# Kernel tuning notes

Measured on AMD Instinct MI355X. Metric: run time of the kernel, lower is better.

## Reference

```python
import jax, jax.numpy as jnp
import numpy as np

EMBED_DIM = 1024
NUM_HEADS = 16
HEAD_DIM = EMBED_DIM // NUM_HEADS
BATCH = 4
SEQ = 2048


def setup_inputs() -> dict:
    key = jax.random.key(0)
    ks = jax.random.split(key, 9)
    s = 1.0 / np.sqrt(EMBED_DIM)
    return {
        "query": jax.random.normal(ks[0], (BATCH, SEQ, EMBED_DIM), jnp.float32),
        "Wq": jax.random.normal(ks[1], (EMBED_DIM, EMBED_DIM), jnp.float32) * s,
        "bq": jnp.zeros((EMBED_DIM,), jnp.float32),
        "Wk": jax.random.normal(ks[2], (EMBED_DIM, EMBED_DIM), jnp.float32) * s,
        "bk": jnp.zeros((EMBED_DIM,), jnp.float32),
        "Wv": jax.random.normal(ks[3], (EMBED_DIM, EMBED_DIM), jnp.float32) * s,
        "bv": jnp.zeros((EMBED_DIM,), jnp.float32),
        "Wo": jax.random.normal(ks[4], (EMBED_DIM, EMBED_DIM), jnp.float32) * s,
        "bo": jnp.zeros((EMBED_DIM,), jnp.float32),
    }


def reference(query, Wq, bq, Wk, bk, Wv, bv, Wo, bo):
    bsz, seq, embed_dim = query.shape
    scaling = HEAD_DIM ** (-0.5)
    # projections (torch Linear: x @ W.T + b)
    q = (query @ Wq.T + bq) * scaling
    k = query @ Wk.T + bk
    v = query @ Wv.T + bv
    # [b, h, s, d]
    q = q.reshape(bsz, seq, NUM_HEADS, HEAD_DIM).transpose(0, 2, 1, 3)
    k = k.reshape(bsz, seq, NUM_HEADS, HEAD_DIM).transpose(0, 2, 1, 3)
    v = v.reshape(bsz, seq, NUM_HEADS, HEAD_DIM).transpose(0, 2, 1, 3)
    # full [b, h, s, s] scores (faithful to the naive original)
    scores = jnp.einsum("bhqd,bhkd->bhqk", q, k)
    causal = jnp.tril(jnp.ones((seq, seq), bool))  # [s, s]
    scores = jnp.where(causal[None, None], scores, -jnp.inf)
    probs = jax.nn.softmax(scores, axis=-1)
    attn = jnp.einsum("bhqk,bhkd->bhqd", probs, v)
    attn = attn.transpose(0, 2, 1, 3).reshape(bsz, seq, embed_dim)
    return attn @ Wo.T + bo
```

## Files before the change

kernel.cpp:

```cpp
#include <hip/hip_runtime.h>
#include <stdint.h>

typedef unsigned short u16;
typedef __attribute__((ext_vector_type(8))) __bf16 bf16x8;
typedef __attribute__((ext_vector_type(4))) float f32x4;

#define SEQL 2048
#define NHEADS 16
#define HDIM 64
#define BSZ 4
#define EMB 1024
#define MROWS (BSZ * SEQL)
#define LOG2E 1.44269504088896f

__device__ __forceinline__ u16 f2bf(float f) {
  union { float f; uint32_t u; } v; v.f = f;
  return (u16)((v.u + 0x7fffu + ((v.u >> 16) & 1u)) >> 16);
}

__device__ __forceinline__ void gload_lds16(const u16* g, u16* l) {
  __builtin_amdgcn_global_load_lds(
      (__attribute__((address_space(1))) void*)(g),
      (__attribute__((address_space(3))) void*)(l), 16, 0, 0);
}

__device__ __forceinline__ void cvt8(const float* __restrict__ in, u16* __restrict__ out, int i) {
  float4 a = *(const float4*)(in + i);
  float4 b = *(const float4*)(in + i + 4);
  uint4 o;
  o.x = f2bf(a.x) | ((uint32_t)f2bf(a.y) << 16);
  o.y = f2bf(a.z) | ((uint32_t)f2bf(a.w) << 16);
  o.z = f2bf(b.x) | ((uint32_t)f2bf(b.y) << 16);
  o.w = f2bf(b.z) | ((uint32_t)f2bf(b.w) << 16);
  *(uint4*)(out + i) = o;
}

__global__ void cvt_kernel(const float* __restrict__ in, u16* __restrict__ out, int n) {
  int i = (blockIdx.x * blockDim.x + threadIdx.x) * 8;
  if (i + 8 <= n) cvt8(in, out, i);
}

__global__ void cvt_w4(const float* __restrict__ w0, const float* __restrict__ w1,
                       const float* __restrict__ w2, const float* __restrict__ w3,
                       u16* __restrict__ o0, u16* __restrict__ o1,
                       u16* __restrict__ o2, u16* __restrict__ o3) {
  const float* in = blockIdx.y == 0 ? w0 : blockIdx.y == 1 ? w1 : blockIdx.y == 2 ? w2 : w3;
  u16* out = blockIdx.y == 0 ? o0 : blockIdx.y == 1 ? o1 : blockIdx.y == 2 ? o2 : o3;
  int i = (blockIdx.x * blockDim.x + threadIdx.x) * 8;
  cvt8(in, out, i);
}

__device__ __forceinline__ void gemm_core(const u16* __restrict__ A, const u16* __restrict__ B,
                                          int m0, int n0, u16* As, u16* Bs, f32x4 acc[4][4]) {
  const int tid = threadIdx.x;
  const int lane = tid & 63;
  const int wid = tid >> 6;
  const int wm = wid >> 1, wn = wid & 1;
  const int srow = lane >> 2;
  const int scol = (lane & 3) * 8;
  const int lrow = lane & 15;
  const int kg = (lane >> 4) * 8;

  const u16* Ag0 = A + (size_t)(m0 + wid * 32 + srow) * EMB + scol;
  const u16* Bg0 = B + (size_t)(n0 + wid * 32 + srow) * EMB + scol;
  u16* Al0 = As + (wid * 32 + srow) * 32 + scol;
  u16* Bl0 = Bs + (wid * 32 + srow) * 32 + scol;

  for (int k0 = 0; k0 < EMB; k0 += 32) {
    gload_lds16(Ag0 + k0, Al0);
    gload_lds16(Ag0 + k0 + 16 * EMB, Al0 + 16 * 32);
    gload_lds16(Bg0 + k0, Bl0);
    gload_lds16(Bg0 + k0 + 16 * EMB, Bl0 + 16 * 32);
    __syncthreads();
    bf16x8 af[4], bfr[4];
#pragma unroll
    for (int f = 0; f < 4; ++f) {
      af[f]  = *(const bf16x8*)(As + (wm * 64 + f * 16 + lrow) * 32 + kg);
      bfr[f] = *(const bf16x8*)(Bs + (wn * 64 + f * 16 + lrow) * 32 + kg);
    }
#pragma unroll
    for (int fm = 0; fm < 4; ++fm)
#pragma unroll
      for (int fn = 0; fn < 4; ++fn)
        acc[fm][fn] = __builtin_amdgcn_mfma_f32_16x16x32_bf16(af[fm], bfr[fn], acc[fm][fn], 0, 0, 0);
    __syncthreads();
  }
}

__global__ __launch_bounds__(256, 2) void gemm_qkv(
    const u16* __restrict__ X,
    const u16* __restrict__ Wq, const u16* __restrict__ Wk, const u16* __restrict__ Wv,
    const float* __restrict__ bq, const float* __restrict__ bk, const float* __restrict__ bv,
    u16* __restrict__ Qb, u16* __restrict__ Kb, u16* __restrict__ Vt) {
  __shared__ u16 As[128 * 32];
  __shared__ u16 Bs[128 * 32];
  const int which = blockIdx.y;
  const u16* W = which == 0 ? Wq : which == 1 ? Wk : Wv;
  const float* bias = which == 0 ? bq : which == 1 ? bk : bv;

  const int mt = blockIdx.x >> 3, nt = blockIdx.x & 7;
  const f32x4 fzero = {0.f, 0.f, 0.f, 0.f};
  f32x4 acc[4][4];
#pragma unroll
  for (int i = 0; i < 4; ++i)
#pragma unroll
    for (int j = 0; j < 4; ++j) acc[i][j] = fzero;

  gemm_core(X, W, mt * 128, nt * 128, As, Bs, acc);

  const int lane = threadIdx.x & 63;
  const int wid = threadIdx.x >> 6;
  const int wm = wid >> 1, wn = wid & 1;
  const int lrow = lane & 15, g = lane >> 4;

  if (which == 2) {
#pragma unroll
    for (int fm = 0; fm < 4; ++fm)
#pragma unroll
      for (int fn = 0; fn < 4; ++fn) {
        int n = nt * 128 + wn * 64 + fn * 16 + lrow;
        float bs = bias[n];
        int h = n >> 6, d = n & 63;
        int m0 = mt * 128 + wm * 64 + fm * 16 + g * 4;
        int b = m0 >> 11, s = m0 & 2047;
        union { u16 s4[4]; uint2 u; } o;
#pragma unroll
        for (int r = 0; r < 4; ++r) o.s4[r] = f2bf(acc[fm][fn][r] + bs);
        *(uint2*)(Vt + ((size_t)(b * NHEADS + h) * HDIM + d) * SEQL + s) = o.u;
      }
  } else {
    u16* Ob = which == 0 ? Qb : Kb;
    const float scale = which == 0 ? 0.125f * LOG2E : 1.0f;
#pragma unroll
    for (int fm = 0; fm < 4; ++fm)
#pragma unroll
      for (int fn = 0; fn < 4; ++fn) {
        int n = nt * 128 + wn * 64 + fn * 16 + lrow;
        float bs = bias[n];
        int h = n >> 6, d = n & 63;
#pragma unroll
        for (int r = 0; r < 4; ++r) {
          int m = mt * 128 + wm * 64 + fm * 16 + g * 4 + r;
          int b = m >> 11, s = m & 2047;
          float v = (acc[fm][fn][r] + bs) * scale;
          Ob[(size_t)((b * NHEADS + h) * SEQL + s) * HDIM + d] = f2bf(v);
        }
      }
  }
}

__global__ __launch_bounds__(256, 2) void gemm_out(
    const u16* __restrict__ Ain, const u16* __restrict__ Wo,
    const float* __restrict__ bo, float* __restrict__ out) {
  __shared__ u16 As[128 * 32];
  __shared__ u16 Bs[128 * 32];
  const int mt = blockIdx.x >> 3, nt = blockIdx.x & 7;
  const f32x4 fzero = {0.f, 0.f, 0.f, 0.f};
  f32x4 acc[4][4];
#pragma unroll
  for (int i = 0; i < 4; ++i)
#pragma unroll
    for (int j = 0; j < 4; ++j) acc[i][j] = fzero;

  gemm_core(Ain, Wo, mt * 128, nt * 128, As, Bs, acc);

  const int lane = threadIdx.x & 63;
  const int wid = threadIdx.x >> 6;
  const int wm = wid >> 1, wn = wid & 1;
  const int lrow = lane & 15, g = lane >> 4;
#pragma unroll
  for (int fm = 0; fm < 4; ++fm)
#pragma unroll
    for (int fn = 0; fn < 4; ++fn) {
      int n = nt * 128 + wn * 64 + fn * 16 + lrow;
      float bs = bo[n];
#pragma unroll
      for (int r = 0; r < 4; ++r) {
        int m = mt * 128 + wm * 64 + fm * 16 + g * 4 + r;
        out[(size_t)m * EMB + n] = acc[fm][fn][r] + bs;
      }
    }
}

__device__ __forceinline__ int swz(int row, int colE) {
  return row * 64 + (colE ^ ((row & 7) << 3));
}

__global__ __launch_bounds__(256, 4) void attn2_kernel(
    const u16* __restrict__ Qb, const u16* __restrict__ Kb, const u16* __restrict__ Vt,
    u16* __restrict__ Ab) {
  __shared__ u16 Ks[2][64 * 64];
  __shared__ u16 Vs[2][64 * 64];

  const int bid = blockIdx.x;
  const int grp = bid >> 6;
  const int bh  = bid & 63;
  const int qt  = (grp & 1) ? (grp >> 1) : (31 - (grp >> 1));
  const int q0  = qt * 64;
  const int NT  = qt + 1;

  const int tid = threadIdx.x, lane = tid & 63, wid = tid >> 6;
  const int lrow = lane & 15, g = lane >> 4, kg = g * 8;

  const u16* Qbh = Qb + (size_t)bh * SEQL * HDIM;
  const u16* Kbh = Kb + (size_t)bh * SEQL * HDIM;
  const u16* Vbh = Vt + (size_t)bh * HDIM * SEQL;

  const int qrow = q0 + wid * 16 + lrow;
  const bf16x8 qf0 = *(const bf16x8*)(Qbh + (size_t)qrow * HDIM + kg);
  const bf16x8 qf1 = *(const bf16x8*)(Qbh + (size_t)qrow * HDIM + 32 + kg);

  const int srow = tid >> 3;
  const int sce  = (tid & 7) * 8;

  float m_run = -1e30f, l_run = 0.f;
  const f32x4 fzero = {0.f, 0.f, 0.f, 0.f};
  f32x4 accO[4];
#pragma unroll
  for (int d = 0; d < 4; ++d) accO[d] = fzero;

  {
    uint4 k0 = *(const uint4*)(Kbh + (size_t)srow * HDIM + sce);
    uint4 k1 = *(const uint4*)(Kbh + (size_t)(srow + 32) * HDIM + sce);
    uint4 v0 = *(const uint4*)(Vbh + (size_t)srow * SEQL + sce);
    uint4 v1 = *(const uint4*)(Vbh + (size_t)(srow + 32) * SEQL + sce);
    *(uint4*)(&Ks[0][swz(srow, sce)]) = k0;
    *(uint4*)(&Ks[0][swz(srow + 32, sce)]) = k1;
    *(uint4*)(&Vs[0][swz(srow, sce)]) = v0;
    *(uint4*)(&Vs[0][swz(srow + 32, sce)]) = v1;
  }
  __syncthreads();

  for (int t = 0; t < NT; ++t) {
    const int cur = t & 1;
    const int kv0 = t * 64;
    const bool pf = (t + 1 < NT);
    uint4 k0, k1, v0, v1;
    if (pf) {
      const int kvn = kv0 + 64;
      k0 = *(const uint4*)(Kbh + (size_t)(kvn + srow) * HDIM + sce);
      k1 = *(const uint4*)(Kbh + (size_t)(kvn + srow + 32) * HDIM + sce);
      v0 = *(const uint4*)(Vbh + (size_t)srow * SEQL + kvn + sce);
      v1 = *(const uint4*)(Vbh + (size_t)(srow + 32) * SEQL + kvn + sce);
    }

    f32x4 sacc[4];
    __builtin_amdgcn_s_setprio(1);
#pragma unroll
    for (int kb = 0; kb < 4; ++kb) {
      bf16x8 kfa = *(const bf16x8*)(&Ks[cur][swz(kb * 16 + lrow, kg)]);
      bf16x8 kfb = *(const bf16x8*)(&Ks[cur][swz(kb * 16 + lrow, 32 + kg)]);
      f32x4 z = fzero;
      z = __builtin_amdgcn_mfma_f32_16x16x32_bf16(kfa, qf0, z, 0, 0, 0);
      z = __builtin_amdgcn_mfma_f32_16x16x32_bf16(kfb, qf1, z, 0, 0, 0);
      sacc[kb] = z;
    }
    __builtin_amdgcn_s_setprio(0);

    if (kv0 + 63 > q0 + wid * 16) {
#pragma unroll
      for (int kb = 0; kb < 4; ++kb)
#pragma unroll
        for (int r = 0; r < 4; ++r)
          if (kv0 + kb * 16 + g * 4 + r > qrow) sacc[kb][r] = -1e30f;
    }

    float mx = sacc[0][0];
#pragma unroll
    for (int kb = 0; kb < 4; ++kb)
#pragma unroll
      for (int r = 0; r < 4; ++r) mx = fmaxf(mx, sacc[kb][r]);
    mx = fmaxf(mx, __shfl_xor(mx, 16));
    mx = fmaxf(mx, __shfl_xor(mx, 32));

    if (!__all(mx <= m_run + 8.f)) {
      const float mnew = fmaxf(m_run, mx);
      const float sc = __builtin_amdgcn_exp2f(m_run - mnew);
      m_run = mnew;
      l_run *= sc;
#pragma unroll
      for (int d = 0; d < 4; ++d) accO[d] *= sc;
    }

    bf16x8 pa[2];
    float ls = 0.f;
#pragma unroll
    for (int kb = 0; kb < 4; ++kb)
#pragma unroll
      for (int r = 0; r < 4; ++r) {
        float p = __builtin_amdgcn_exp2f(sacc[kb][r] - m_run);
        ls += p;
        pa[kb >> 1][(kb & 1) * 4 + r] = (__bf16)p;
      }
    l_run += ls;

    __builtin_amdgcn_s_setprio(1);
#pragma unroll
    for (int ks = 0; ks < 2; ++ks)
#pragma unroll
      for (int d = 0; d < 4; ++d) {
        union { ushort4 h[2]; bf16x8 v; } vf;
        vf.h[0] = *(const ushort4*)(&Vs[cur][swz(d * 16 + lrow, ks * 32 + g * 4)]);
        vf.h[1] = *(const ushort4*)(&Vs[cur][swz(d * 16 + lrow, ks * 32 + 16 + g * 4)]);
        accO[d] = __builtin_amdgcn_mfma_f32_16x16x32_bf16(vf.v, pa[ks], accO[d], 0, 0, 0);
      }
    __builtin_amdgcn_s_setprio(0);

    if (pf) {
      const int nb = cur ^ 1;
      *(uint4*)(&Ks[nb][swz(srow, sce)]) = k0;
      *(uint4*)(&Ks[nb][swz(srow + 32, sce)]) = k1;
      *(uint4*)(&Vs[nb][swz(srow, sce)]) = v0;
      *(uint4*)(&Vs[nb][swz(srow + 32, sce)]) = v1;
    }
    __syncthreads();
  }

  float l = l_run;
  l += __shfl_xor(l, 16);
  l += __shfl_xor(l, 32);
  const float inv = 1.f / l;
  const int b = bh >> 4, h = bh & 15;
#pragma unroll
  for (int d = 0; d < 4; ++d) {
    union { u16 s4[4]; uint2 u; } o;
#pragma unroll
    for (int r = 0; r < 4; ++r) o.s4[r] = f2bf(accO[d][r] * inv);
    *(uint2*)(Ab + (size_t)(b * SEQL + qrow) * EMB + h * HDIM + d * 16 + g * 4) = o.u;
  }
}

extern "C" void kernel_launch(void* const* d_in, const int* in_sizes, int n_in,
                              void* d_out, int out_size, void* d_ws, size_t ws_size,
                              hipStream_t stream) {
  (void)in_sizes; (void)n_in; (void)out_size; (void)ws_size;
  const float* query = (const float*)d_in[0];
  const float* Wq = (const float*)d_in[1];
  const float* bq = (const float*)d_in[2];
  const float* Wk = (const float*)d_in[3];
  const float* bk = (const float*)d_in[4];
  const float* Wv = (const float*)d_in[5];
  const float* bv = (const float*)d_in[6];
  const float* Wo = (const float*)d_in[7];
  const float* bo = (const float*)d_in[8];
  float* out = (float*)d_out;

  const size_t MB = 1u << 20;
  char* ws = (char*)d_ws;
  u16* Xb  = (u16*)(ws);
  u16* Wqb = (u16*)(ws + 16 * MB);
  u16* Wkb = (u16*)(ws + 18 * MB);
  u16* Wvb = (u16*)(ws + 20 * MB);
  u16* Wob = (u16*)(ws + 22 * MB);
  u16* Qbf = (u16*)(ws + 24 * MB);
  u16* Kbf = (u16*)(ws + 40 * MB);
  u16* Vtg = (u16*)(ws + 56 * MB);
  u16* Ab  = Xb;

  cvt_kernel<<<4096, 256, 0, stream>>>(query, Xb, MROWS * EMB);
  cvt_w4<<<dim3(512, 4), 256, 0, stream>>>(Wq, Wk, Wv, Wo, Wqb, Wkb, Wvb, Wob);
  gemm_qkv<<<dim3(512, 3), 256, 0, stream>>>(Xb, Wqb, Wkb, Wvb, bq, bk, bv, Qbf, Kbf, Vtg);
  attn2_kernel<<<2048, 256, 0, stream>>>(Qbf, Kbf, Vtg, Ab);
  gemm_out<<<512, 256, 0, stream>>>(Ab, Wob, bo, out);
}
```

Before: 191.7 us.

## Use 128-wide KV tiles in attention and merge conversion kernels into one launch

The attention kernel now processes 128 keys per iteration with a single LDS buffer instead of double-buffered 64-key tiles. This halves the loop iterations and barriers per pass and widens each softmax step, at the cost of more registers, an extra barrier around the LDS refill, and wasted masked work on the diagonal tile for odd query tiles. The two bf16 conversion kernels for activations and weights are also fused into one launch, which relies on the four weight buffers being contiguous in the workspace.

```diff
diff --git a/kernel.cpp b/kernel.cpp
--- a/kernel.cpp
+++ b/kernel.cpp
@@ -35,19 +35,21 @@
   *(uint4*)(out + i) = o;
 }
 
-__global__ void cvt_kernel(const float* __restrict__ in, u16* __restrict__ out, int n) {
+#define XN (MROWS * EMB)
+__global__ void cvt_all(const float* __restrict__ query,
+                        const float* __restrict__ w0, const float* __restrict__ w1,
+                        const float* __restrict__ w2, const float* __restrict__ w3,
+                        u16* __restrict__ Xb, u16* __restrict__ Wqb) {
   int i = (blockIdx.x * blockDim.x + threadIdx.x) * 8;
-  if (i + 8 <= n) cvt8(in, out, i);
-}
-
-__global__ void cvt_w4(const float* __restrict__ w0, const float* __restrict__ w1,
-                       const float* __restrict__ w2, const float* __restrict__ w3,
-                       u16* __restrict__ o0, u16* __restrict__ o1,
-                       u16* __restrict__ o2, u16* __restrict__ o3) {
-  const float* in = blockIdx.y == 0 ? w0 : blockIdx.y == 1 ? w1 : blockIdx.y == 2 ? w2 : w3;
-  u16* out = blockIdx.y == 0 ? o0 : blockIdx.y == 1 ? o1 : blockIdx.y == 2 ? o2 : o3;
-  int i = (blockIdx.x * blockDim.x + threadIdx.x) * 8;
-  cvt8(in, out, i);
+  if (i < XN) {
+    cvt8(query, Xb, i);
+  } else {
+    int j = i - XN;
+    int w = j >> 20;
+    int jj = j & 1048575;
+    const float* src = w == 0 ? w0 : w == 1 ? w1 : w == 2 ? w2 : w3;
+    cvt8(src, Wqb + ((size_t)w << 20), jj);
+  }
 }
 
 __device__ __forceinline__ void gemm_core(const u16* __restrict__ A, const u16* __restrict__ B,
@@ -182,22 +184,25 @@
     }
 }
 
-__device__ __forceinline__ int swz(int row, int colE) {
+__device__ __forceinline__ int swzK(int row, int colE) {
   return row * 64 + (colE ^ ((row & 7) << 3));
 }
-
-__global__ __launch_bounds__(256, 4) void attn2_kernel(
+__device__ __forceinline__ int swzV(int row, int colE) {
+  return row * 128 + (colE ^ ((row & 7) << 3));
+}
+
+__global__ __launch_bounds__(256, 4) void attn3_kernel(
     const u16* __restrict__ Qb, const u16* __restrict__ Kb, const u16* __restrict__ Vt,
     u16* __restrict__ Ab) {
-  __shared__ u16 Ks[2][64 * 64];
-  __shared__ u16 Vs[2][64 * 64];
+  __shared__ u16 Ks[128 * 64];
+  __shared__ u16 Vs[64 * 128];
 
   const int bid = blockIdx.x;
   const int grp = bid >> 6;
   const int bh  = bid & 63;
   const int qt  = (grp & 1) ? (grp >> 1) : (31 - (grp >> 1));
   const int q0  = qt * 64;
-  const int NT  = qt + 1;
+  const int NT  = (qt + 2) >> 1;
 
   const int tid = threadIdx.x, lane = tid & 63, wid = tid >> 6;
   const int lrow = lane & 15, g = lane >> 4, kg = g * 8;
@@ -210,8 +215,8 @@
   const bf16x8 qf0 = *(const bf16x8*)(Qbh + (size_t)qrow * HDIM + kg);
   const bf16x8 qf1 = *(const bf16x8*)(Qbh + (size_t)qrow * HDIM + 32 + kg);
 
-  const int srow = tid >> 3;
-  const int sce  = (tid & 7) * 8;
+  const int kr = tid >> 3, kc = (tid & 7) * 8;
+  const int vr = tid >> 4, vc = (tid & 15) * 8;
 
   float m_run = -1e30f, l_run = 0.f;
   const f32x4 fzero = {0.f, 0.f, 0.f, 0.f};
@@ -219,37 +224,34 @@
 #pragma unroll
   for (int d = 0; d < 4; ++d) accO[d] = fzero;
 
-  {
-    uint4 k0 = *(const uint4*)(Kbh + (size_t)srow * HDIM + sce);
-    uint4 k1 = *(const uint4*)(Kbh + (size_t)(srow + 32) * HDIM + sce);
-    uint4 v0 = *(const uint4*)(Vbh + (size_t)srow * SEQL + sce);
-    uint4 v1 = *(const uint4*)(Vbh + (size_t)(srow + 32) * SEQL + sce);
-    *(uint4*)(&Ks[0][swz(srow, sce)]) = k0;
-    *(uint4*)(&Ks[0][swz(srow + 32, sce)]) = k1;
-    *(uint4*)(&Vs[0][swz(srow, sce)]) = v0;
-    *(uint4*)(&Vs[0][swz(srow + 32, sce)]) = v1;
+#pragma unroll
+  for (int i = 0; i < 4; ++i) {
+    uint4 kk = *(const uint4*)(Kbh + (size_t)(kr + i * 32) * HDIM + kc);
+    *(uint4*)(&Ks[swzK(kr + i * 32, kc)]) = kk;
+    uint4 vv = *(const uint4*)(Vbh + (size_t)(vr + i * 16) * SEQL + vc);
+    *(uint4*)(&Vs[swzV(vr + i * 16, vc)]) = vv;
   }
   __syncthreads();
 
   for (int t = 0; t < NT; ++t) {
-    const int cur = t & 1;
-    const int kv0 = t * 64;
+    const int kv0 = t * 128;
     const bool pf = (t + 1 < NT);
-    uint4 k0, k1, v0, v1;
+    uint4 pk[4], pv[4];
     if (pf) {
-      const int kvn = kv0 + 64;
-      k0 = *(const uint4*)(Kbh + (size_t)(kvn + srow) * HDIM + sce);
-      k1 = *(const uint4*)(Kbh + (size_t)(kvn + srow + 32) * HDIM + sce);
-      v0 = *(const uint4*)(Vbh + (size_t)srow * SEQL + kvn + sce);
-      v1 = *(const uint4*)(Vbh + (size_t)(srow + 32) * SEQL + kvn + sce);
-    }
-
-    f32x4 sacc[4];
+      const int kvn = kv0 + 128;
+#pragma unroll
+      for (int i = 0; i < 4; ++i) {
+        pk[i] = *(const uint4*)(Kbh + (size_t)(kvn + kr + i * 32) * HDIM + kc);
+        pv[i] = *(const uint4*)(Vbh + (size_t)(vr + i * 16) * SEQL + kvn + vc);
+      }
+    }
+
+    f32x4 sacc[8];
     __builtin_amdgcn_s_setprio(1);
 #pragma unroll
-    for (int kb = 0; kb < 4; ++kb) {
-      bf16x8 kfa = *(const bf16x8*)(&Ks[cur][swz(kb * 16 + lrow, kg)]);
-      bf16x8 kfb = *(const bf16x8*)(&Ks[cur][swz(kb * 16 + lrow, 32 + kg)]);
+    for (int kb = 0; kb < 8; ++kb) {
+      bf16x8 kfa = *(const bf16x8*)(&Ks[swzK(kb * 16 + lrow, kg)]);
+      bf16x8 kfb = *(const bf16x8*)(&Ks[swzK(kb * 16 + lrow, 32 + kg)]);
       f32x4 z = fzero;
       z = __builtin_amdgcn_mfma_f32_16x16x32_bf16(kfa, qf0, z, 0, 0, 0);
       z = __builtin_amdgcn_mfma_f32_16x16x32_bf16(kfb, qf1, z, 0, 0, 0);
@@ -257,9 +259,9 @@
     }
     __builtin_amdgcn_s_setprio(0);
 
-    if (kv0 + 63 > q0 + wid * 16) {
-#pragma unroll
-      for (int kb = 0; kb < 4; ++kb)
+    if (kv0 + 127 > q0 + wid * 16) {
+#pragma unroll
+      for (int kb = 0; kb < 8; ++kb)
 #pragma unroll
         for (int r = 0; r < 4; ++r)
           if (kv0 + kb * 16 + g * 4 + r > qrow) sacc[kb][r] = -1e30f;
@@ -267,7 +269,7 @@
 
     float mx = sacc[0][0];
 #pragma unroll
-    for (int kb = 0; kb < 4; ++kb)
+    for (int kb = 0; kb < 8; ++kb)
 #pragma unroll
       for (int r = 0; r < 4; ++r) mx = fmaxf(mx, sacc[kb][r]);
     mx = fmaxf(mx, __shfl_xor(mx, 16));
@@ -282,10 +284,10 @@
       for (int d = 0; d < 4; ++d) accO[d] *= sc;
     }
 
-    bf16x8 pa[2];
+    bf16x8 pa[4];
     float ls = 0.f;
 #pragma unroll
-    for (int kb = 0; kb < 4; ++kb)
+    for (int kb = 0; kb < 8; ++kb)
 #pragma unroll
       for (int r = 0; r < 4; ++r) {
         float p = __builtin_amdgcn_exp2f(sacc[kb][r] - m_run);
@@ -296,24 +298,25 @@
 
     __builtin_amdgcn_s_setprio(1);
 #pragma unroll
-    for (int ks = 0; ks < 2; ++ks)
+    for (int ks = 0; ks < 4; ++ks)
 #pragma unroll
       for (int d = 0; d < 4; ++d) {
         union { ushort4 h[2]; bf16x8 v; } vf;
-        vf.h[0] = *(const ushort4*)(&Vs[cur][swz(d * 16 + lrow, ks * 32 + g * 4)]);
-        vf.h[1] = *(const ushort4*)(&Vs[cur][swz(d * 16 + lrow, ks * 32 + 16 + g * 4)]);
+        vf.h[0] = *(const ushort4*)(&Vs[swzV(d * 16 + lrow, ks * 32 + g * 4)]);
+        vf.h[1] = *(const ushort4*)(&Vs[swzV(d * 16 + lrow, ks * 32 + 16 + g * 4)]);
         accO[d] = __builtin_amdgcn_mfma_f32_16x16x32_bf16(vf.v, pa[ks], accO[d], 0, 0, 0);
       }
     __builtin_amdgcn_s_setprio(0);
 
     if (pf) {
-      const int nb = cur ^ 1;
-      *(uint4*)(&Ks[nb][swz(srow, sce)]) = k0;
-      *(uint4*)(&Ks[nb][swz(srow + 32, sce)]) = k1;
-      *(uint4*)(&Vs[nb][swz(srow, sce)]) = v0;
-      *(uint4*)(&Vs[nb][swz(srow + 32, sce)]) = v1;
-    }
-    __syncthreads();
+      __syncthreads();
+#pragma unroll
+      for (int i = 0; i < 4; ++i) {
+        *(uint4*)(&Ks[swzK(kr + i * 32, kc)]) = pk[i];
+        *(uint4*)(&Vs[swzV(vr + i * 16, vc)]) = pv[i];
+      }
+      __syncthreads();
+    }
   }
 
   float l = l_run;
@@ -357,9 +360,8 @@
   u16* Vtg = (u16*)(ws + 56 * MB);
   u16* Ab  = Xb;
 
-  cvt_kernel<<<4096, 256, 0, stream>>>(query, Xb, MROWS * EMB);
-  cvt_w4<<<dim3(512, 4), 256, 0, stream>>>(Wq, Wk, Wv, Wo, Wqb, Wkb, Wvb, Wob);
+  cvt_all<<<6144, 256, 0, stream>>>(query, Wq, Wk, Wv, Wo, Xb, Wqb);
   gemm_qkv<<<dim3(512, 3), 256, 0, stream>>>(Xb, Wqb, Wkb, Wvb, bq, bk, bv, Qbf, Kbf, Vtg);
-  attn2_kernel<<<2048, 256, 0, stream>>>(Qbf, Kbf, Vtg, Ab);
+  attn3_kernel<<<2048, 256, 0, stream>>>(Qbf, Kbf, Vtg, Ab);
   gemm_out<<<512, 256, 0, stream>>>(Ab, Wob, bo, out);
 }
```

Result: slower. 290.6 us (+51.6%).

## Pair causal query tiles per attention block and merge conversion kernels

Applied to the files above, without the earlier changes.

Each attention block now handles two query tiles in sequence, tile qa and tile 31-qa, so every block does the same total number of KV iterations. The grid shrinks from 2048 to 1024 blocks, which removes the causal load imbalance and tail effect of the per-tile scheduling. The separate input and weight bf16 conversion kernels are also merged into one launch. This relies on the four converted weight buffers sitting contiguously in the workspace. The trade-off is fewer resident blocks to hide latency and an extra barrier between the two phases.

```diff
diff --git a/kernel.cpp b/kernel.cpp
--- a/kernel.cpp
+++ b/kernel.cpp
@@ -35,19 +35,21 @@
   *(uint4*)(out + i) = o;
 }
 
-__global__ void cvt_kernel(const float* __restrict__ in, u16* __restrict__ out, int n) {
+#define XN (MROWS * EMB)
+__global__ void cvt_all(const float* __restrict__ query,
+                        const float* __restrict__ w0, const float* __restrict__ w1,
+                        const float* __restrict__ w2, const float* __restrict__ w3,
+                        u16* __restrict__ Xb, u16* __restrict__ Wqb) {
   int i = (blockIdx.x * blockDim.x + threadIdx.x) * 8;
-  if (i + 8 <= n) cvt8(in, out, i);
-}
-
-__global__ void cvt_w4(const float* __restrict__ w0, const float* __restrict__ w1,
-                       const float* __restrict__ w2, const float* __restrict__ w3,
-                       u16* __restrict__ o0, u16* __restrict__ o1,
-                       u16* __restrict__ o2, u16* __restrict__ o3) {
-  const float* in = blockIdx.y == 0 ? w0 : blockIdx.y == 1 ? w1 : blockIdx.y == 2 ? w2 : w3;
-  u16* out = blockIdx.y == 0 ? o0 : blockIdx.y == 1 ? o1 : blockIdx.y == 2 ? o2 : o3;
-  int i = (blockIdx.x * blockDim.x + threadIdx.x) * 8;
-  cvt8(in, out, i);
+  if (i < XN) {
+    cvt8(query, Xb, i);
+  } else {
+    int j = i - XN;
+    int w = j >> 20;
+    int jj = j & 1048575;
+    const float* src = w == 0 ? w0 : w == 1 ? w1 : w == 2 ? w2 : w3;
+    cvt8(src, Wqb + ((size_t)w << 20), jj);
+  }
 }
 
 __device__ __forceinline__ void gemm_core(const u16* __restrict__ A, const u16* __restrict__ B,
@@ -186,18 +188,15 @@
   return row * 64 + (colE ^ ((row & 7) << 3));
 }
 
-__global__ __launch_bounds__(256, 4) void attn2_kernel(
+__global__ __launch_bounds__(256, 4) void attn4_kernel(
     const u16* __restrict__ Qb, const u16* __restrict__ Kb, const u16* __restrict__ Vt,
     u16* __restrict__ Ab) {
   __shared__ u16 Ks[2][64 * 64];
   __shared__ u16 Vs[2][64 * 64];
 
   const int bid = blockIdx.x;
-  const int grp = bid >> 6;
+  const int qa  = bid >> 6;
   const int bh  = bid & 63;
-  const int qt  = (grp & 1) ? (grp >> 1) : (31 - (grp >> 1));
-  const int q0  = qt * 64;
-  const int NT  = qt + 1;
 
   const int tid = threadIdx.x, lane = tid & 63, wid = tid >> 6;
   const int lrow = lane & 15, g = lane >> 4, kg = g * 8;
@@ -206,127 +205,136 @@
   const u16* Kbh = Kb + (size_t)bh * SEQL * HDIM;
   const u16* Vbh = Vt + (size_t)bh * HDIM * SEQL;
 
-  const int qrow = q0 + wid * 16 + lrow;
-  const bf16x8 qf0 = *(const bf16x8*)(Qbh + (size_t)qrow * HDIM + kg);
-  const bf16x8 qf1 = *(const bf16x8*)(Qbh + (size_t)qrow * HDIM + 32 + kg);
-
   const int srow = tid >> 3;
   const int sce  = (tid & 7) * 8;
 
-  float m_run = -1e30f, l_run = 0.f;
   const f32x4 fzero = {0.f, 0.f, 0.f, 0.f};
-  f32x4 accO[4];
-#pragma unroll
-  for (int d = 0; d < 4; ++d) accO[d] = fzero;
-
-  {
-    uint4 k0 = *(const uint4*)(Kbh + (size_t)srow * HDIM + sce);
-    uint4 k1 = *(const uint4*)(Kbh + (size_t)(srow + 32) * HDIM + sce);
-    uint4 v0 = *(const uint4*)(Vbh + (size_t)srow * SEQL + sce);
-    uint4 v1 = *(const uint4*)(Vbh + (size_t)(srow + 32) * SEQL + sce);
-    *(uint4*)(&Ks[0][swz(srow, sce)]) = k0;
-    *(uint4*)(&Ks[0][swz(srow + 32, sce)]) = k1;
-    *(uint4*)(&Vs[0][swz(srow, sce)]) = v0;
-    *(uint4*)(&Vs[0][swz(srow + 32, sce)]) = v1;
-  }
-  __syncthreads();
-
-  for (int t = 0; t < NT; ++t) {
-    const int cur = t & 1;
-    const int kv0 = t * 64;
-    const bool pf = (t + 1 < NT);
-    uint4 k0, k1, v0, v1;
-    if (pf) {
-      const int kvn = kv0 + 64;
-      k0 = *(const uint4*)(Kbh + (size_t)(kvn + srow) * HDIM + sce);
-      k1 = *(const uint4*)(Kbh + (size_t)(kvn + srow + 32) * HDIM + sce);
-      v0 = *(const uint4*)(Vbh + (size_t)srow * SEQL + kvn + sce);
-      v1 = *(const uint4*)(Vbh + (size_t)(srow + 32) * SEQL + kvn + sce);
-    }
-
-    f32x4 sacc[4];
-    __builtin_amdgcn_s_setprio(1);
-#pragma unroll
-    for (int kb = 0; kb < 4; ++kb) {
-      bf16x8 kfa = *(const bf16x8*)(&Ks[cur][swz(kb * 16 + lrow, kg)]);
-      bf16x8 kfb = *(const bf16x8*)(&Ks[cur][swz(kb * 16 + lrow, 32 + kg)]);
-      f32x4 z = fzero;
-      z = __builtin_amdgcn_mfma_f32_16x16x32_bf16(kfa, qf0, z, 0, 0, 0);
-      z = __builtin_amdgcn_mfma_f32_16x16x32_bf16(kfb, qf1, z, 0, 0, 0);
-      sacc[kb] = z;
-    }
-    __builtin_amdgcn_s_setprio(0);
-
-    if (kv0 + 63 > q0 + wid * 16) {
+  const int b = bh >> 4, h = bh & 15;
+
+#pragma unroll 1
+  for (int ph = 0; ph < 2; ++ph) {
+    const int qt = ph ? (31 - qa) : qa;
+    const int q0 = qt * 64;
+    const int NT = qt + 1;
+
+    const int qrow = q0 + wid * 16 + lrow;
+    const bf16x8 qf0 = *(const bf16x8*)(Qbh + (size_t)qrow * HDIM + kg);
+    const bf16x8 qf1 = *(const bf16x8*)(Qbh + (size_t)qrow * HDIM + 32 + kg);
+
+    float m_run = -1e30f, l_run = 0.f;
+    f32x4 accO[4];
+#pragma unroll
+    for (int d = 0; d < 4; ++d) accO[d] = fzero;
+
+    {
+      uint4 k0 = *(const uint4*)(Kbh + (size_t)srow * HDIM + sce);
+      uint4 k1 = *(const uint4*)(Kbh + (size_t)(srow + 32) * HDIM + sce);
+      uint4 v0 = *(const uint4*)(Vbh + (size_t)srow * SEQL + sce);
+      uint4 v1 = *(const uint4*)(Vbh + (size_t)(srow + 32) * SEQL + sce);
+      *(uint4*)(&Ks[0][swz(srow, sce)]) = k0;
+      *(uint4*)(&Ks[0][swz(srow + 32, sce)]) = k1;
+      *(uint4*)(&Vs[0][swz(srow, sce)]) = v0;
+      *(uint4*)(&Vs[0][swz(srow + 32, sce)]) = v1;
+    }
+    __syncthreads();
+
+    for (int t = 0; t < NT; ++t) {
+      const int cur = t & 1;
+      const int kv0 = t * 64;
+      const bool pf = (t + 1 < NT);
+      uint4 k0, k1, v0, v1;
+      if (pf) {
+        const int kvn = kv0 + 64;
+        k0 = *(const uint4*)(Kbh + (size_t)(kvn + srow) * HDIM + sce);
+        k1 = *(const uint4*)(Kbh + (size_t)(kvn + srow + 32) * HDIM + sce);
+        v0 = *(const uint4*)(Vbh + (size_t)srow * SEQL + kvn + sce);
+        v1 = *(const uint4*)(Vbh + (size_t)(srow + 32) * SEQL + kvn + sce);
+      }
+
+      f32x4 sacc[4];
+      __builtin_amdgcn_s_setprio(1);
+#pragma unroll
+      for (int kb = 0; kb < 4; ++kb) {
+        bf16x8 kfa = *(const bf16x8*)(&Ks[cur][swz(kb * 16 + lrow, kg)]);
+        bf16x8 kfb = *(const bf16x8*)(&Ks[cur][swz(kb * 16 + lrow, 32 + kg)]);
+        f32x4 z = fzero;
+        z = __builtin_amdgcn_mfma_f32_16x16x32_bf16(kfa, qf0, z, 0, 0, 0);
+        z = __builtin_amdgcn_mfma_f32_16x16x32_bf16(kfb, qf1, z, 0, 0, 0);
+        sacc[kb] = z;
+      }
+      __builtin_amdgcn_s_setprio(0);
+
+      if (kv0 + 63 > q0 + wid * 16) {
+#pragma unroll
+        for (int kb = 0; kb < 4; ++kb)
+#pragma unroll
+          for (int r = 0; r < 4; ++r)
+            if (kv0 + kb * 16 + g * 4 + r > qrow) sacc[kb][r] = -1e30f;
+      }
+
+      float mx = sacc[0][0];
 #pragma unroll
       for (int kb = 0; kb < 4; ++kb)
 #pragma unroll
-        for (int r = 0; r < 4; ++r)
-          if (kv0 + kb * 16 + g * 4 + r > qrow) sacc[kb][r] = -1e30f;
-    }
-
-    float mx = sacc[0][0];
-#pragma unroll
-    for (int kb = 0; kb < 4; ++kb)
-#pragma unroll
-      for (int r = 0; r < 4; ++r) mx = fmaxf(mx, sacc[kb][r]);
-    mx = fmaxf(mx, __shfl_xor(mx, 16));
-    mx = fmaxf(mx, __shfl_xor(mx, 32));
-
-    if (!__all(mx <= m_run + 8.f)) {
-      const float mnew = fmaxf(m_run, mx);
-      const float sc = __builtin_amdgcn_exp2f(m_run - mnew);
-      m_run = mnew;
-      l_run *= sc;
-#pragma unroll
-      for (int d = 0; d < 4; ++d) accO[d] *= sc;
-    }
-
-    bf16x8 pa[2];
-    float ls = 0.f;
-#pragma unroll
-    for (int kb = 0; kb < 4; ++kb)
-#pragma unroll
-      for (int r = 0; r < 4; ++r) {
-        float p = __builtin_amdgcn_exp2f(sacc[kb][r] - m_run);
-        ls += p;
-        pa[kb >> 1][(kb & 1) * 4 + r] = (__bf16)p;
-      }
-    l_run += ls;
-
-    __builtin_amdgcn_s_setprio(1);
-#pragma unroll
-    for (int ks = 0; ks < 2; ++ks)
-#pragma unroll
-      for (int d = 0; d < 4; ++d) {
-        union { ushort4 h[2]; bf16x8 v; } vf;
-        vf.h[0] = *(const ushort4*)(&Vs[cur][swz(d * 16 + lrow, ks * 32 + g * 4)]);
-        vf.h[1] = *(const ushort4*)(&Vs[cur][swz(d * 16 + lrow, ks * 32 + 16 + g * 4)]);
-        accO[d] = __builtin_amdgcn_mfma_f32_16x16x32_bf16(vf.v, pa[ks], accO[d], 0, 0, 0);
-      }
-    __builtin_amdgcn_s_setprio(0);
-
-    if (pf) {
-      const int nb = cur ^ 1;
-      *(uint4*)(&Ks[nb][swz(srow, sce)]) = k0;
-      *(uint4*)(&Ks[nb][swz(srow + 32, sce)]) = k1;
-      *(uint4*)(&Vs[nb][swz(srow, sce)]) = v0;
-      *(uint4*)(&Vs[nb][swz(srow + 32, sce)]) = v1;
+        for (int r = 0; r < 4; ++r) mx = fmaxf(mx, sacc[kb][r]);
+      mx = fmaxf(mx, __shfl_xor(mx, 16));
+      mx = fmaxf(mx, __shfl_xor(mx, 32));
+
+      if (!__all(mx <= m_run + 8.f)) {
+        const float mnew = fmaxf(m_run, mx);
+        const float sc = __builtin_amdgcn_exp2f(m_run - mnew);
+        m_run = mnew;
+        l_run *= sc;
+#pragma unroll
+        for (int d = 0; d < 4; ++d) accO[d] *= sc;
+      }
+
+      bf16x8 pa[2];
+      float ls = 0.f;
+#pragma unroll
+      for (int kb = 0; kb < 4; ++kb)
+#pragma unroll
+        for (int r = 0; r < 4; ++r) {
+          float p = __builtin_amdgcn_exp2f(sacc[kb][r] - m_run);
+          ls += p;
+          pa[kb >> 1][(kb & 1) * 4 + r] = (__bf16)p;
+        }
+      l_run += ls;
+
+      __builtin_amdgcn_s_setprio(1);
+#pragma unroll
+      for (int ks = 0; ks < 2; ++ks)
+#pragma unroll
+        for (int d = 0; d < 4; ++d) {
+          union { ushort4 h[2]; bf16x8 v; } vf;
+          vf.h[0] = *(const ushort4*)(&Vs[cur][swz(d * 16 + lrow, ks * 32 + g * 4)]);
+          vf.h[1] = *(const ushort4*)(&Vs[cur][swz(d * 16 + lrow, ks * 32 + 16 + g * 4)]);
+          accO[d] = __builtin_amdgcn_mfma_f32_16x16x32_bf16(vf.v, pa[ks], accO[d], 0, 0, 0);
+        }
+      __builtin_amdgcn_s_setprio(0);
+
+      if (pf) {
+        const int nb = cur ^ 1;
+        *(uint4*)(&Ks[nb][swz(srow, sce)]) = k0;
+        *(uint4*)(&Ks[nb][swz(srow + 32, sce)]) = k1;
+        *(uint4*)(&Vs[nb][swz(srow, sce)]) = v0;
+        *(uint4*)(&Vs[nb][swz(srow + 32, sce)]) = v1;
+      }
+      __syncthreads();
+    }
+
+    float l = l_run;
+    l += __shfl_xor(l, 16);
+    l += __shfl_xor(l, 32);
+    const float inv = 1.f / l;
+#pragma unroll
+    for (int d = 0; d < 4; ++d) {
+      union { u16 s4[4]; uint2 u; } o;
+#pragma unroll
+      for (int r = 0; r < 4; ++r) o.s4[r] = f2bf(accO[d][r] * inv);
+      *(uint2*)(Ab + (size_t)(b * SEQL + qrow) * EMB + h * HDIM + d * 16 + g * 4) = o.u;
     }
     __syncthreads();
-  }
-
-  float l = l_run;
-  l += __shfl_xor(l, 16);
-  l += __shfl_xor(l, 32);
-  const float inv = 1.f / l;
-  const int b = bh >> 4, h = bh & 15;
-#pragma unroll
-  for (int d = 0; d < 4; ++d) {
-    union { u16 s4[4]; uint2 u; } o;
-#pragma unroll
-    for (int r = 0; r < 4; ++r) o.s4[r] = f2bf(accO[d][r] * inv);
-    *(uint2*)(Ab + (size_t)(b * SEQL + qrow) * EMB + h * HDIM + d * 16 + g * 4) = o.u;
   }
 }
 
@@ -357,9 +365,8 @@
   u16* Vtg = (u16*)(ws + 56 * MB);
   u16* Ab  = Xb;
 
-  cvt_kernel<<<4096, 256, 0, stream>>>(query, Xb, MROWS * EMB);
-  cvt_w4<<<dim3(512, 4), 256, 0, stream>>>(Wq, Wk, Wv, Wo, Wqb, Wkb, Wvb, Wob);
+  cvt_all<<<6144, 256, 0, stream>>>(query, Wq, Wk, Wv, Wo, Xb, Wqb);
   gemm_qkv<<<dim3(512, 3), 256, 0, stream>>>(Xb, Wqb, Wkb, Wvb, bq, bk, bv, Qbf, Kbf, Vtg);
-  attn2_kernel<<<2048, 256, 0, stream>>>(Qbf, Kbf, Vtg, Ab);
+  attn4_kernel<<<1024, 256, 0, stream>>>(Qbf, Kbf, Vtg, Ab);
   gemm_out<<<512, 256, 0, stream>>>(Ab, Wob, bo, out);
 }
```

After: 181.5 us. 1.06x faster.
